# Performance work log

Hardware: AMD Instinct MI355X
Metric: run time of the kernel (lower is better)

The kernel has to match this reference:

```python
import jax, jax.numpy as jnp
import numpy as np

N = 8192  # dimension; degree = 2


def setup_inputs() -> dict:
    key = jax.random.key(0)
    k1, k2 = jax.random.split(key)
    num_coeffs = N + N * (N - 1) // 2  # sum_{k=1..2} C(N,k)
    return {
        "input": jax.random.normal(k1, (N,), dtype=jnp.float32),
        "coeffs": jax.random.normal(k2, (num_coeffs,), dtype=jnp.float32),
    }


def reference(input, coeffs):
    # Hamiltonian polynomial: sum over all 1- and 2-subsets of variables,
    # terms ordered [deg-1 terms (lex), deg-2 terms (lex)] to match
    # torch.combinations concatenation order, then dotted with coeffs.
    n = input.shape[0]
    # np.triu_indices(k=1) enumerates (i,j) with i<j in row-major (lex) order,
    # exactly matching torch.combinations(x, r=2).
    iu0, iu1 = np.triu_indices(n, k=1)
    terms1 = input                      # [n]
    terms2 = input[iu0] * input[iu1]    # [C(n,2)] pairwise products
    terms = jnp.concatenate([terms1, terms2])
    return terms @ coeffs
```

## Files before the change

kernel.cpp:

```cpp
#include <hip/hip_runtime.h>
#include <cstdint>

#define N 8192
#define BLK 512
#define NBLK 1024


__device__ __forceinline__ float row_partial(const float* __restrict__ c2,
                                             const float (&xs)[4][2048],
                                             int O, int L, int i) {
    const int t = threadIdx.x;
    const float* cp = c2 + O;
    const int xb0 = i + 1;
    float s = 0.0f;

    int pro = (4 - (O & 3)) & 3;
    if (pro > L) pro = L;
    if (t < pro) {
        const int xi = xb0 + t;
        s += cp[t] * xs[xi & 3][xi >> 2];
    }

    const int R = L - pro;
    const int V = R >> 2;
    const int tail = R & 3;
    const float4* __restrict__ cv = (const float4*)(cp + pro);
    const int xb = xb0 + pro;

    for (int v = t; v < V; v += BLK) {
        const float4 c = cv[v];
        const int xi = xb + (v << 2);
        const float x0 = xs[xi & 3][xi >> 2];
        const float x1 = xs[(xi + 1) & 3][(xi + 1) >> 2];
        const float x2 = xs[(xi + 2) & 3][(xi + 2) >> 2];
        const float x3 = xs[(xi + 3) & 3][(xi + 3) >> 2];
        s += c.x * x0 + c.y * x1 + c.z * x2 + c.w * x3;
    }
    if (t < tail) {
        const int e = (V << 2) + t;
        const int xi = xb + e;
        s += cp[pro + e] * xs[xi & 3][xi >> 2];
    }
    return s;
}

__global__ __launch_bounds__(BLK) void ham_main(const float* __restrict__ x,
                                                const float* __restrict__ coeffs,
                                                float* __restrict__ ws) {
    __shared__ float xs[4][2048];
    const int t = threadIdx.x;
    const int b = blockIdx.x;
    const float* __restrict__ c1 = coeffs;
    const float* __restrict__ c2 = coeffs + N;

    {
        const float4* __restrict__ x4 = (const float4*)x;
        for (int k = t; k < 2048; k += BLK) {
            const float4 v = x4[k];
            xs[0][k] = v.x; xs[1][k] = v.y; xs[2][k] = v.z; xs[3][k] = v.w;
        }
    }
    __syncthreads();

    float acc = 0.0f;

    #pragma unroll
    for (int pp = 0; pp < 4; ++pp) {
        const int p = b + pp * NBLK;
        const int i1 = p;
        const int O1 = (i1 * (2 * N - i1 - 1)) >> 1;
        acc += xs[i1 & 3][i1 >> 2] * row_partial(c2, xs, O1, N - 1 - i1, i1);

        const int i2 = N - 2 - p;
        if (i2 > i1) {
            const int O2 = (i2 * (2 * N - i2 - 1)) >> 1;
            acc += xs[i2 & 3][i2 >> 2] * row_partial(c2, xs, O2, N - 1 - i2, i2);
        }
    }

    if (t < 8) {
        const int g = (b << 3) + t;
        acc += c1[g] * xs[g & 3][g >> 2];
    }

    #pragma unroll
    for (int o = 32; o > 0; o >>= 1) acc += __shfl_down(acc, o, 64);
    __shared__ float smem[BLK / 64];
    const int wave = t >> 6;
    const int lane = t & 63;
    if (lane == 0) smem[wave] = acc;
    __syncthreads();
    if (t == 0) {
        float v = 0.0f;
        #pragma unroll
        for (int w = 0; w < BLK / 64; ++w) v += smem[w];
        ws[b] = v;
    }
}

__global__ __launch_bounds__(256) void ham_reduce(const float* __restrict__ ws,
                                                  float* __restrict__ out) {
    const int t = threadIdx.x;
    const float4* __restrict__ w4 = (const float4*)ws;
    const float4 v4 = w4[t];
    float v = v4.x + v4.y + v4.z + v4.w;
    #pragma unroll
    for (int o = 32; o > 0; o >>= 1) v += __shfl_down(v, o, 64);
    __shared__ float smem[4];
    const int wave = t >> 6;
    const int lane = t & 63;
    if (lane == 0) smem[wave] = v;
    __syncthreads();
    if (t == 0) out[0] = smem[0] + smem[1] + smem[2] + smem[3];
}

extern "C" void kernel_launch(void* const* d_in, const int* in_sizes, int n_in,
                              void* d_out, int out_size, void* d_ws, size_t ws_size,
                              hipStream_t stream) {
    const float* x      = (const float*)d_in[0];
    const float* coeffs = (const float*)d_in[1];
    float* out = (float*)d_out;
    float* ws  = (float*)d_ws;

    ham_main<<<NBLK, BLK, 0, stream>>>(x, coeffs, ws);
    ham_main<<<NBLK, BLK, 0, stream>>>(x, coeffs, ws);
    ham_reduce<<<1, 256, 0, stream>>>(ws, out);
}
```

Baseline: 225.9 us.

## Drop duplicate main launch and batch row coefficient loads before compute

Removes the second, redundant launch of the main kernel so the coefficient array is streamed only once. The per-row strided loop is replaced by a fixed unrolled scheme where each thread issues all four float4 coefficient loads for both paired rows before doing the shared-memory dot products. A launch-bounds occupancy hint is added. This raises memory-level parallelism at the cost of more registers and clamped dummy loads for masked lanes.

```diff
diff --git a/kernel.cpp b/kernel.cpp
--- a/kernel.cpp
+++ b/kernel.cpp
@@ -4,60 +4,28 @@
 #define N 8192
 #define BLK 512
 #define NBLK 1024
+#define C2_LEN 33550336
+#define C2_QUADS (C2_LEN / 4)
 
 
-__device__ __forceinline__ float row_partial(const float* __restrict__ c2,
-                                             const float (&xs)[4][2048],
-                                             int O, int L, int i) {
-    const int t = threadIdx.x;
-    const float* cp = c2 + O;
-    const int xb0 = i + 1;
-    float s = 0.0f;
-
-    int pro = (4 - (O & 3)) & 3;
-    if (pro > L) pro = L;
-    if (t < pro) {
-        const int xi = xb0 + t;
-        s += cp[t] * xs[xi & 3][xi >> 2];
-    }
-
-    const int R = L - pro;
-    const int V = R >> 2;
-    const int tail = R & 3;
-    const float4* __restrict__ cv = (const float4*)(cp + pro);
-    const int xb = xb0 + pro;
-
-    for (int v = t; v < V; v += BLK) {
-        const float4 c = cv[v];
-        const int xi = xb + (v << 2);
-        const float x0 = xs[xi & 3][xi >> 2];
-        const float x1 = xs[(xi + 1) & 3][(xi + 1) >> 2];
-        const float x2 = xs[(xi + 2) & 3][(xi + 2) >> 2];
-        const float x3 = xs[(xi + 3) & 3][(xi + 3) >> 2];
-        s += c.x * x0 + c.y * x1 + c.z * x2 + c.w * x3;
-    }
-    if (t < tail) {
-        const int e = (V << 2) + t;
-        const int xi = xb + e;
-        s += cp[pro + e] * xs[xi & 3][xi >> 2];
-    }
-    return s;
-}
-
-__global__ __launch_bounds__(BLK) void ham_main(const float* __restrict__ x,
-                                                const float* __restrict__ coeffs,
-                                                float* __restrict__ ws) {
+__global__ __launch_bounds__(BLK, 4) void ham_main(const float* __restrict__ x,
+                                                   const float* __restrict__ coeffs,
+                                                   float* __restrict__ ws) {
     __shared__ float xs[4][2048];
+    __shared__ float smem[BLK / 64];
     const int t = threadIdx.x;
     const int b = blockIdx.x;
     const float* __restrict__ c1 = coeffs;
     const float* __restrict__ c2 = coeffs + N;
+    const float4* __restrict__ cq = (const float4*)c2;
 
     {
         const float4* __restrict__ x4 = (const float4*)x;
-        for (int k = t; k < 2048; k += BLK) {
-            const float4 v = x4[k];
-            xs[0][k] = v.x; xs[1][k] = v.y; xs[2][k] = v.z; xs[3][k] = v.w;
+        #pragma unroll
+        for (int k = 0; k < 4; ++k) {
+            const int m = t + k * BLK;
+            const float4 v = x4[m];
+            xs[0][m] = v.x; xs[1][m] = v.y; xs[2][m] = v.z; xs[3][m] = v.w;
         }
     }
     __syncthreads();
@@ -66,16 +34,70 @@
 
     #pragma unroll
     for (int pp = 0; pp < 4; ++pp) {
-        const int p = b + pp * NBLK;
+        const int p  = b + pp * NBLK;
         const int i1 = p;
+        const int i2 = N - 2 - p;
+        const bool hasB = (i2 > i1);
+
         const int O1 = (i1 * (2 * N - i1 - 1)) >> 1;
-        acc += xs[i1 & 3][i1 >> 2] * row_partial(c2, xs, O1, N - 1 - i1, i1);
+        const int L1 = N - 1 - i1;
+        int pro1 = (4 - (O1 & 3)) & 3; if (pro1 > L1) pro1 = L1;
+        const int R1 = L1 - pro1, V1 = R1 >> 2, tl1 = R1 & 3;
+        const int q1 = (O1 + pro1) >> 2;
+        const int xbA = i1 + 1 + pro1;
 
-        const int i2 = N - 2 - p;
-        if (i2 > i1) {
-            const int O2 = (i2 * (2 * N - i2 - 1)) >> 1;
-            acc += xs[i2 & 3][i2 >> 2] * row_partial(c2, xs, O2, N - 1 - i2, i2);
+        int O2 = 0, pro2 = 0, V2 = 0, tl2 = 0, q2 = 0, xbB = i2 + 1;
+        if (hasB) {
+            O2 = (i2 * (2 * N - i2 - 1)) >> 1;
+            const int L2 = N - 1 - i2;
+            pro2 = (4 - (O2 & 3)) & 3; if (pro2 > L2) pro2 = L2;
+            const int R2 = L2 - pro2; V2 = R2 >> 2; tl2 = R2 & 3;
+            q2 = (O2 + pro2) >> 2;
+            xbB = i2 + 1 + pro2;
         }
+
+        float4 ca[4], cb[4];
+        int xia[4], xib[4];
+        #pragma unroll
+        for (int k = 0; k < 4; ++k) {
+            const int idx = t + k * BLK;
+            const bool mA = idx < V1;
+            const int iA = mA ? idx : 0;
+            ca[k] = cq[q1 + iA];
+            if (!mA) ca[k] = make_float4(0.f, 0.f, 0.f, 0.f);
+            xia[k] = min(xbA + (iA << 2), N - 4);
+
+            const bool mB = idx < V2;
+            const int iB = mB ? idx : 0;
+            int qb = q2 + iB; qb = min(qb, C2_QUADS - 1);
+            cb[k] = cq[qb];
+            if (!mB) cb[k] = make_float4(0.f, 0.f, 0.f, 0.f);
+            xib[k] = min(xbB + (iB << 2), N - 4);
+        }
+
+        float sA = 0.0f, sB = 0.0f;
+        if (t < pro1) { const int xi = i1 + 1 + t;            sA += c2[O1 + t] * xs[xi & 3][xi >> 2]; }
+        if (t < tl1)  { const int e = (V1 << 2) + t; const int xi = xbA + e; sA += c2[O1 + pro1 + e] * xs[xi & 3][xi >> 2]; }
+        if (t < pro2) { const int xi = i2 + 1 + t;            sB += c2[O2 + t] * xs[xi & 3][xi >> 2]; }
+        if (t < tl2)  { const int e = (V2 << 2) + t; const int xi = xbB + e; sB += c2[O2 + pro2 + e] * xs[xi & 3][xi >> 2]; }
+
+        #pragma unroll
+        for (int k = 0; k < 4; ++k) {
+            const int a0 = xia[k];
+            sA += ca[k].x * xs[a0 & 3][a0 >> 2]
+                + ca[k].y * xs[(a0 + 1) & 3][(a0 + 1) >> 2]
+                + ca[k].z * xs[(a0 + 2) & 3][(a0 + 2) >> 2]
+                + ca[k].w * xs[(a0 + 3) & 3][(a0 + 3) >> 2];
+            const int b0 = xib[k];
+            sB += cb[k].x * xs[b0 & 3][b0 >> 2]
+                + cb[k].y * xs[(b0 + 1) & 3][(b0 + 1) >> 2]
+                + cb[k].z * xs[(b0 + 2) & 3][(b0 + 2) >> 2]
+                + cb[k].w * xs[(b0 + 3) & 3][(b0 + 3) >> 2];
+        }
+
+        const float xA = xs[i1 & 3][i1 >> 2];
+        const float xB = hasB ? xs[i2 & 3][i2 >> 2] : 0.0f;
+        acc += xA * sA + xB * sB;
     }
 
     if (t < 8) {
@@ -85,7 +107,6 @@
 
     #pragma unroll
     for (int o = 32; o > 0; o >>= 1) acc += __shfl_down(acc, o, 64);
-    __shared__ float smem[BLK / 64];
     const int wave = t >> 6;
     const int lane = t & 63;
     if (lane == 0) smem[wave] = acc;
@@ -123,6 +144,5 @@
     float* ws  = (float*)d_ws;
 
     ham_main<<<NBLK, BLK, 0, stream>>>(x, coeffs, ws);
-    ham_main<<<NBLK, BLK, 0, stream>>>(x, coeffs, ws);
     ham_reduce<<<1, 256, 0, stream>>>(ws, out);
 }
```

Result: slower. 324.7 us (+43.7%).
